# Kernel optimization log

Hardware: AMD Instinct MI355X
Metric: run time of the kernel (lower is better)

## Reference

```python
import jax, jax.numpy as jnp
import numpy as np

N, E, G = 50000, 1600000, 64
XDIM, HID, NF, NG, GDIM, NL = 32, 128, 128, 50, 16, 6
CUTOFF = 10.0
SHID = 64
EPS = 1e-5

_offset = jnp.linspace(0.0, CUTOFF, NG)
_coeff = -0.5 / float((CUTOFF / (NG - 1)) ** 2)


def _bn(h, g, b):
    m = h.mean(axis=0)
    v = h.var(axis=0)
    return (h - m) * jax.lax.rsqrt(v + EPS) * g + b


def setup_inputs() -> dict:
    key = jax.random.key(0)
    ks = jax.random.split(key, 48)

    def w(k, shape):
        fan = shape[-2] if len(shape) >= 2 else shape[-1]
        return (jax.random.normal(k, shape, jnp.float32) / np.sqrt(fan)).astype(jnp.float32)

    inp = {
        "x": jax.random.normal(ks[0], (N, XDIM), jnp.float32),
        "edge_index": jax.random.randint(ks[1], (2, E), 0, N, dtype=jnp.int32).astype(jnp.int64),
        "edge_attr": jax.random.normal(ks[2], (E, 3), jnp.float32),
        "batch": jnp.sort(jax.random.randint(ks[3], (N,), 0, G, dtype=jnp.int32)).astype(jnp.int64),
        "u": jax.random.normal(ks[4], (G, GDIM), jnp.float32),
        # node encoder MLP: lin -> bn -> relu -> lin
        "We1": w(ks[5], (XDIM, HID)), "be1": jnp.zeros(HID), "ge1": jnp.ones(HID), "bte1": jnp.zeros(HID),
        "We2": w(ks[6], (HID, HID)), "be2": jnp.zeros(HID),
        # 6 stacked interactions
        "Wf1": w(ks[7], (NL, NG, NF)), "bf1": jnp.zeros((NL, NF)),
        "Wf2": w(ks[8], (NL, NF, NF)), "bf2": jnp.zeros((NL, NF)),
        "Wd1": w(ks[9], (NL, HID, HID)), "bd1": jnp.zeros((NL, HID)),
        "Wd2": w(ks[10], (NL, HID, HID)), "bd2": jnp.zeros((NL, HID)),
        # global MLP: lin -> bn -> relu -> lin
        "Wg1": w(ks[11], (GDIM, HID)), "bg1": jnp.zeros(HID), "gg1": jnp.ones(HID), "btg1": jnp.zeros(HID),
        "Wg2": w(ks[12], (HID, HID)), "bg2": jnp.zeros(HID),
        # shift predictor: [2*HID, 64, 64, 1]
        "Ws1": w(ks[13], (2 * HID, SHID)), "bs1": jnp.zeros(SHID), "gs1": jnp.ones(SHID), "bts1": jnp.zeros(SHID),
        "Ws2": w(ks[14], (SHID, SHID)), "bs2": jnp.zeros(SHID), "gs2": jnp.ones(SHID), "bts2": jnp.zeros(SHID),
        "Ws3": w(ks[15], (SHID, 1)), "bs3": jnp.zeros(1),
    }
    return inp


def reference(x, edge_index, edge_attr, batch, u,
              We1, be1, ge1, bte1, We2, be2,
              Wf1, bf1, Wf2, bf2, Wd1, bd1, Wd2, bd2,
              Wg1, bg1, gg1, btg1, Wg2, bg2,
              Ws1, bs1, gs1, bts1, Ws2, bs2, gs2, bts2, Ws3, bs3):
    row = edge_index[0]  # source j
    col = edge_index[1]  # target i

    # node encoder
    h = jax.nn.relu(_bn(x @ We1 + be1, ge1, bte1)) @ We2 + be2  # [N,HID]

    # gaussian smearing of edge lengths
    d = jnp.linalg.norm(edge_attr, axis=1)  # [E]
    ea = jnp.exp(_coeff * jnp.square(d[:, None] - _offset[None, :]))  # [E,NG]

    for l in range(NL):
        W = jax.nn.relu(ea @ Wf1[l] + bf1[l]) @ Wf2[l] + bf2[l]  # [E,NF]
        msg = h[row] * W                                          # gather + elementwise
        agg = jax.ops.segment_sum(msg, col, num_segments=N)       # scatter-add
        h = h + (jax.nn.relu(agg @ Wd1[l] + bd1[l]) @ Wd2[l] + bd2[l])

    # global MLP
    u_p = jax.nn.relu(_bn(u @ Wg1 + bg1, gg1, btg1)) @ Wg2 + bg2  # [G,HID]

    # shift predictor on [h, u_p[batch]]
    s = jnp.concatenate([h, u_p[batch]], axis=1)  # [N,2*HID]
    s = jax.nn.relu(_bn(s @ Ws1 + bs1, gs1, bts1))
    s = jax.nn.relu(_bn(s @ Ws2 + bs2, gs2, bts2))
    shifts = s @ Ws3 + bs3  # [N,1]
    return shifts, h, ea, u_p
```

## Files before the change

kernel.cpp:

```cpp
#include <hip/hip_runtime.h>

#define NN 50000
#define NE 1600000
#define NGR 64
#define XD 32
#define HID 128
#define NF 128
#define NG 50
#define GD 16
#define NL 6
#define SH 64
#define EPSF 1e-5f
#define TBL 4096
#define INVSTEP 320.0f

typedef __bf16 bf16_t;
typedef bf16_t bf16x8 __attribute__((ext_vector_type(8)));
typedef float f32x4 __attribute__((ext_vector_type(4)));

__device__ __forceinline__ unsigned pack_bf2(float a, float b) {
  unsigned short ua = __builtin_bit_cast(unsigned short, (bf16_t)a);
  unsigned short ub = __builtin_bit_cast(unsigned short, (bf16_t)b);
  return (unsigned)ua | ((unsigned)ub << 16);
}
__device__ __forceinline__ float bflo(unsigned u) { return __uint_as_float(u << 16); }
__device__ __forceinline__ float bfhi(unsigned u) { return __uint_as_float(u & 0xffff0000u); }
__device__ __forceinline__ float blerp(unsigned u, float fr) {
  float w0 = bflo(u), w1 = bfhi(u);
  return fmaf(fr, w1 - w0, w0);
}

__global__ __launch_bounds__(256) void k_hist(const int* __restrict__ col,
                                              int* __restrict__ hist) {
  for (int e = blockIdx.x * 256 + threadIdx.x; e < NE; e += gridDim.x * 256)
    atomicAdd(&hist[col[e]], 1);
}

__global__ __launch_bounds__(1024) void k_scan(int* __restrict__ hist,
                                               int* __restrict__ rowptr) {
  const int tid = threadIdx.x;
  const int CH = 49;
  const int base = tid * CH;
  int s = 0;
  for (int i = 0; i < CH; ++i) {
    int idx = base + i;
    if (idx < NN) s += hist[idx];
  }
  __shared__ int part[1024];
  part[tid] = s;
  __syncthreads();
  for (int off = 1; off < 1024; off <<= 1) {
    int v = (tid >= off) ? part[tid - off] : 0;
    __syncthreads();
    part[tid] += v;
    __syncthreads();
  }
  int run = part[tid] - s;
  for (int i = 0; i < CH; ++i) {
    int idx = base + i;
    if (idx < NN) {
      int c = hist[idx];
      rowptr[idx] = run;
      hist[idx] = run;
      run += c;
    }
  }
  if (tid == 0) rowptr[NN] = NE;
}

__global__ __launch_bounds__(256) void k_scatter2(const int* __restrict__ col,
    const int* __restrict__ row, const float* __restrict__ eattr,
    int* __restrict__ cursor, uint2* __restrict__ metap) {
  for (int e = blockIdx.x * 256 + threadIdx.x; e < NE; e += gridDim.x * 256) {
    float ax = eattr[(size_t)e * 3], ay = eattr[(size_t)e * 3 + 1], az = eattr[(size_t)e * 3 + 2];
    float d = sqrtf(ax * ax + ay * ay + az * az);
    float tt = fminf(d * INVSTEP, (float)(TBL - 2) + 0.999f);
    int id = (int)tt;
    int c = col[e];
    int pos = atomicAdd(&cursor[c], 1);
    unsigned mw = ((unsigned)row[e] << 16) | ((unsigned)id << 4) | (unsigned)(c & 15);
    metap[pos] = make_uint2(mw, __float_as_uint(tt - (float)id));
  }
}

__global__ __launch_bounds__(128) void k_tabbuild3(
    const float* __restrict__ Wf1, const float* __restrict__ bf1,
    const float* __restrict__ Wf2, const float* __restrict__ bf2,
    unsigned int* __restrict__ tabp) {
  const int bid = blockIdx.x;
  const int l = bid / (TBL / 8);
  const int t0 = (bid - l * (TBL / 8)) * 8;
  const int c = threadIdx.x;
  __shared__ float g_s[9][NG];
  __shared__ float f1_s[9][NF];
  for (int i = c; i < 9 * NG; i += 128) {
    int kk = i / NG, g = i - kk * NG;
    int t = min(t0 + kk, TBL - 1);
    float d = (float)t * (1.0f / INVSTEP);
    float z = d - 0.2040816327f * (float)g;
    g_s[kk][g] = expf(-12.005f * z * z);
  }
  __syncthreads();
  const float* W1 = Wf1 + (size_t)l * NG * NF;
  float f1r[9];
#pragma unroll
  for (int kk = 0; kk < 9; ++kk) f1r[kk] = bf1[(size_t)l * NF + c];
  for (int g = 0; g < NG; ++g) {
    float w = W1[g * NF + c];
#pragma unroll
    for (int kk = 0; kk < 9; ++kk) f1r[kk] = fmaf(g_s[kk][g], w, f1r[kk]);
  }
#pragma unroll
  for (int kk = 0; kk < 9; ++kk) f1_s[kk][c] = fmaxf(f1r[kk], 0.f);
  __syncthreads();
  const float* W2 = Wf2 + (size_t)l * NF * NF;
  float outr[9];
#pragma unroll
  for (int kk = 0; kk < 9; ++kk) outr[kk] = bf2[(size_t)l * NF + c];
  for (int k = 0; k < NF; ++k) {
    float w = W2[k * NF + c];
#pragma unroll
    for (int kk = 0; kk < 9; ++kk) outr[kk] = fmaf(f1_s[kk][k], w, outr[kk]);
  }
#pragma unroll
  for (int kk = 0; kk < 8; ++kk)
    tabp[((size_t)l * TBL + t0 + kk) * NF + c] = pack_bf2(outr[kk], outr[kk + 1]);
}

__global__ __launch_bounds__(256) void k_prepw(const float* __restrict__ Wd1,
    const float* __restrict__ Wd2,
    bf16_t* __restrict__ Wd1Thi, bf16_t* __restrict__ Wd1Tlo,
    bf16_t* __restrict__ Wd2Thi, bf16_t* __restrict__ Wd2Tlo) {
  const int S1 = NL * 128 * 128;
  int idx = blockIdx.x * 256 + threadIdx.x;
  if (idx < 2 * S1) {
    int which = idx / S1;
    int jj = idx - which * S1;
    int l = jj / (128 * 128);
    int r = jj - l * (128 * 128);
    int c = r >> 7, k = r & 127;
    const float* W = (which == 0) ? Wd1 : Wd2;
    float v = W[(size_t)l * 128 * 128 + (size_t)k * 128 + c];
    bf16_t hv = (bf16_t)v;
    bf16_t lv = (bf16_t)(v - (float)hv);
    if (which == 0) { Wd1Thi[jj] = hv; Wd1Tlo[jj] = lv; }
    else            { Wd2Thi[jj] = hv; Wd2Tlo[jj] = lv; }
  }
}

__global__ __launch_bounds__(256) void k_enc1(const float* __restrict__ x,
    const float* __restrict__ We1, const float* __restrict__ be1,
    float* __restrict__ t, float* __restrict__ stats) {
  int c = threadIdx.x & 127;
  int half = threadIdx.x >> 7;
  float b = be1[c];
  float psum = 0.f, psq = 0.f;
  for (int n = blockIdx.x * 2 + half; n < NN; n += gridDim.x * 2) {
    const float* xr = x + (size_t)n * XD;
    float v = b;
#pragma unroll
    for (int k = 0; k < XD; ++k) v = fmaf(xr[k], We1[k * HID + c], v);
    t[(size_t)n * HID + c] = v;
    psum += v; psq += v * v;
  }
  __shared__ float s0[256], s1[256];
  s0[threadIdx.x] = psum; s1[threadIdx.x] = psq;
  __syncthreads();
  if (threadIdx.x < 128) {
    atomicAdd(&stats[threadIdx.x], s0[threadIdx.x] + s0[threadIdx.x + 128]);
    atomicAdd(&stats[128 + threadIdx.x], s1[threadIdx.x] + s1[threadIdx.x + 128]);
  }
}

__global__ __launch_bounds__(128) void k_bn_fin(const float* __restrict__ gamma,
    const float* __restrict__ beta, float* __restrict__ stats, int C, float invn) {
  int c = threadIdx.x;
  if (c < C) {
    float mean = stats[c] * invn;
    float var = stats[128 + c] * invn - mean * mean;
    float a = gamma[c] * rsqrtf(var + EPSF);
    stats[256 + c] = a;
    stats[384 + c] = beta[c] - mean * a;
  }
}

__global__ __launch_bounds__(128) void k_enc2(const float* __restrict__ t,
    const float* __restrict__ stats, const float* __restrict__ We2,
    const float* __restrict__ be2, float* __restrict__ h,
    unsigned int* __restrict__ hbf) {
  __shared__ float r[HID];
  int c = threadIdx.x;
  float a = stats[256 + c], b = stats[384 + c];
  float bias = be2[c];
  for (int n = blockIdx.x; n < NN; n += gridDim.x) {
    float v = fmaf(t[(size_t)n * HID + c], a, b);
    r[c] = fmaxf(v, 0.f);
    __syncthreads();
    float acc = bias;
#pragma unroll 8
    for (int k = 0; k < HID; ++k) acc = fmaf(r[k], We2[k * HID + c], acc);
    h[(size_t)n * HID + c] = acc;
    float o = __shfl_down(acc, 1);
    if ((c & 1) == 0) hbf[(size_t)n * 64 + (c >> 1)] = pack_bf2(acc, o);
    __syncthreads();
  }
}

__global__ __launch_bounds__(256) void k_smear(const float* __restrict__ eattr,
    float* __restrict__ ea) {
  int idx = blockIdx.x * 256 + threadIdx.x;
  if (idx >= NE * (NG / 2)) return;
  int e = idx / (NG / 2);
  int g0 = (idx - e * (NG / 2)) * 2;
  float ax = eattr[(size_t)e * 3], ay = eattr[(size_t)e * 3 + 1], az = eattr[(size_t)e * 3 + 2];
  float d = sqrtf(ax * ax + ay * ay + az * az);
  float z0 = d - 0.2040816327f * (float)g0;
  float z1 = d - 0.2040816327f * (float)(g0 + 1);
  float2 v = make_float2(__expf(-12.005f * z0 * z0), __expf(-12.005f * z1 * z1));
  *(float2*)(ea + (size_t)e * NG + g0) = v;
}

__global__ __launch_bounds__(256) void k_layer(
    const uint2* __restrict__ metap, const int* __restrict__ rowptr,
    const float* __restrict__ hin, const unsigned int* __restrict__ hbf,
    const unsigned int* __restrict__ tabp,
    const bf16_t* __restrict__ Wd1Thi, const bf16_t* __restrict__ Wd1Tlo,
    const bf16_t* __restrict__ Wd2Thi, const bf16_t* __restrict__ Wd2Tlo,
    const float* __restrict__ bd1, const float* __restrict__ bd2,
    float* __restrict__ hout, unsigned int* __restrict__ hbfo) {
  __shared__ __align__(16) char up[8704];
  float (*agg_s)[HID] = (float(*)[HID])up;
  bf16_t (*t1hi)[136] = (bf16_t(*)[136])up;
  bf16_t (*t1lo)[136] = (bf16_t(*)[136])(up + 4352);
  __shared__ __align__(16) bf16_t ahi_s[16][136];
  __shared__ __align__(16) bf16_t alo_s[16][136];

  const int tid = threadIdx.x;
  const int lane = tid & 63;
  const int w = tid >> 6;
  const int half = lane >> 5;
  const int c0 = (lane & 31) * 4;
  const int hoff = c0 >> 1;
  const int nb = blockIdx.x * 16;
  const int eS = rowptr[nb], eE = rowptr[nb + 16];

  for (int i = tid; i < 16 * HID; i += 256) ((float*)agg_s)[i] = 0.f;
  __syncthreads();

  {
    const int Q = (eE - eS + 3) >> 2;
    int e = eS + w * Q;
    const int wE = min(e + Q, eE);

    float a0 = 0.f, a1 = 0.f, a2 = 0.f, a3 = 0.f;
    int cur = -1;

    auto flush = [&]() {
      if (cur >= 0) {
        atomicAdd(&agg_s[cur][c0], a0);
        atomicAdd(&agg_s[cur][c0 + 1], a1);
        atomicAdd(&agg_s[cur][c0 + 2], a2);
        atomicAdd(&agg_s[cur][c0 + 3], a3);
      }
    };
    auto pbody = [&](const uint2& m, const uint2& hv, const uint4& tv) {
      float fr = __uint_as_float(m.y);
      int dst = m.x & 0xF;
      float m0 = blerp(tv.x, fr) * bflo(hv.x);
      float m1 = blerp(tv.y, fr) * bfhi(hv.x);
      float m2 = blerp(tv.z, fr) * bflo(hv.y);
      float m3 = blerp(tv.w, fr) * bfhi(hv.y);
      if (dst != cur) {
        flush();
        cur = dst; a0 = m0; a1 = m1; a2 = m2; a3 = m3;
      } else {
        a0 += m0; a1 += m1; a2 += m2; a3 += m3;
      }
    };
    auto loadd = [&](const uint2& m, uint2& hv, uint4& tv) {
      hv = *(const uint2*)(hbf + (size_t)(m.x >> 16) * 64 + hoff);
      tv = *(const uint4*)(tabp + (size_t)((m.x >> 4) & 0xFFFu) * HID + c0);
    };

    if (wE - e >= 8) {
      uint2 m0a = metap[e + half], m0b = metap[e + 2 + half];
      uint2 hv0a, hv0b; uint4 tv0a, tv0b;
      loadd(m0a, hv0a, tv0a); loadd(m0b, hv0b, tv0b);
      int ep = e + 4;
      uint2 m1a = metap[ep + half], m1b = metap[ep + 2 + half];
      while (true) {
        const bool more = (ep + 8 <= wE);
        uint2 hv1a, hv1b; uint4 tv1a, tv1b;
        loadd(m1a, hv1a, tv1a); loadd(m1b, hv1b, tv1b);
        uint2 m2a, m2b;
        if (more) { m2a = metap[ep + 4 + half]; m2b = metap[ep + 6 + half]; }
        pbody(m0a, hv0a, tv0a);
        pbody(m0b, hv0b, tv0b);
        if (!more) {
          pbody(m1a, hv1a, tv1a);
          pbody(m1b, hv1b, tv1b);
          ep += 4;
          break;
        }
        m0a = m1a; m0b = m1b;
        hv0a = hv1a; hv0b = hv1b; tv0a = tv1a; tv0b = tv1b;
        m1a = m2a; m1b = m2b;
        ep += 4;
      }
      e = ep;
    }
    for (; e < wE; e += 2) {
      int le = e + half;
      bool valid = le < wE;
      uint2 m = metap[valid ? le : (wE - 1)];
      uint2 hv; uint4 tv;
      loadd(m, hv, tv);
      if (valid) pbody(m, hv, tv);
    }
    flush();
  }
  __syncthreads();

  for (int i = tid; i < 16 * 128; i += 256) {
    int r = i >> 7, k = i & 127;
    float v = agg_s[r][k];
    bf16_t hv = (bf16_t)v;
    ahi_s[r][k] = hv;
    alo_s[r][k] = (bf16_t)(v - (float)hv);
  }
  __syncthreads();

  const int lm = lane & 15;
  const int lk = lane >> 4;
  const int colb = w * 32;
  const int k0base = lk * 8;

  f32x4 acc1g[2];
  acc1g[0] = (f32x4){0.f, 0.f, 0.f, 0.f};
  acc1g[1] = (f32x4){0.f, 0.f, 0.f, 0.f};
#pragma unroll
  for (int s = 0; s < 4; ++s) {
    int k0 = s * 32 + k0base;
    bf16x8 Ahi = *(const bf16x8*)&ahi_s[lm][k0];
    bf16x8 Alo = *(const bf16x8*)&alo_s[lm][k0];
#pragma unroll
    for (int cf = 0; cf < 2; ++cf) {
      int cc = colb + cf * 16 + lm;
      bf16x8 Bh = *(const bf16x8*)(Wd1Thi + (size_t)cc * 128 + k0);
      bf16x8 Bl = *(const bf16x8*)(Wd1Tlo + (size_t)cc * 128 + k0);
      acc1g[cf] = __builtin_amdgcn_mfma_f32_16x16x32_bf16(Ahi, Bh, acc1g[cf], 0, 0, 0);
      acc1g[cf] = __builtin_amdgcn_mfma_f32_16x16x32_bf16(Ahi, Bl, acc1g[cf], 0, 0, 0);
      acc1g[cf] = __builtin_amdgcn_mfma_f32_16x16x32_bf16(Alo, Bh, acc1g[cf], 0, 0, 0);
    }
  }
#pragma unroll
  for (int cf = 0; cf < 2; ++cf) {
    int cc = colb + cf * 16 + lm;
    float bias1 = bd1[cc];
#pragma unroll
    for (int j = 0; j < 4; ++j) {
      int r = lk * 4 + j;
      float v = fmaxf(acc1g[cf][j] + bias1, 0.f);
      bf16_t hv = (bf16_t)v;
      t1hi[r][cc] = hv;
      t1lo[r][cc] = (bf16_t)(v - (float)hv);
    }
  }
  __syncthreads();

  f32x4 acc2g[2];
  acc2g[0] = (f32x4){0.f, 0.f, 0.f, 0.f};
  acc2g[1] = (f32x4){0.f, 0.f, 0.f, 0.f};
#pragma unroll
  for (int s = 0; s < 4; ++s) {
    int k0 = s * 32 + k0base;
    bf16x8 Ahi = *(const bf16x8*)&t1hi[lm][k0];
    bf16x8 Alo = *(const bf16x8*)&t1lo[lm][k0];
#pragma unroll
    for (int cf = 0; cf < 2; ++cf) {
      int cc = colb + cf * 16 + lm;
      bf16x8 Bh = *(const bf16x8*)(Wd2Thi + (size_t)cc * 128 + k0);
      bf16x8 Bl = *(const bf16x8*)(Wd2Tlo + (size_t)cc * 128 + k0);
      acc2g[cf] = __builtin_amdgcn_mfma_f32_16x16x32_bf16(Ahi, Bh, acc2g[cf], 0, 0, 0);
      acc2g[cf] = __builtin_amdgcn_mfma_f32_16x16x32_bf16(Ahi, Bl, acc2g[cf], 0, 0, 0);
      acc2g[cf] = __builtin_amdgcn_mfma_f32_16x16x32_bf16(Alo, Bh, acc2g[cf], 0, 0, 0);
    }
  }
#pragma unroll
  for (int cf = 0; cf < 2; ++cf) {
    int cc = colb + cf * 16 + lm;
    float bias2 = bd2[cc];
#pragma unroll
    for (int j = 0; j < 4; ++j) {
      int r = nb + lk * 4 + j;
      float val = hin[(size_t)r * HID + cc] + acc2g[cf][j] + bias2;
      hout[(size_t)r * HID + cc] = val;
      float o = __shfl_xor(val, 1);
      if ((lm & 1) == 0) hbfo[(size_t)r * 64 + (cc >> 1)] = pack_bf2(val, o);
    }
  }
}

__global__ __launch_bounds__(128) void k_global(const float* __restrict__ u,
    const float* __restrict__ Wg1, const float* __restrict__ bg1,
    const float* __restrict__ gg1, const float* __restrict__ btg1,
    const float* __restrict__ Wg2, const float* __restrict__ bg2,
    float* __restrict__ u_p) {
  __shared__ float t_s[NGR][HID];
  int c = threadIdx.x;
  for (int g = 0; g < NGR; ++g) {
    float v = bg1[c];
#pragma unroll
    for (int k = 0; k < GD; ++k) v = fmaf(u[(size_t)g * GD + k], Wg1[k * HID + c], v);
    t_s[g][c] = v;
  }
  float sum = 0.f, sq = 0.f;
  for (int g = 0; g < NGR; ++g) { float v = t_s[g][c]; sum += v; sq += v * v; }
  float mean = sum * (1.f / NGR);
  float var = sq * (1.f / NGR) - mean * mean;
  float a = gg1[c] * rsqrtf(var + EPSF);
  float b = btg1[c] - mean * a;
  for (int g = 0; g < NGR; ++g) t_s[g][c] = fmaxf(fmaf(t_s[g][c], a, b), 0.f);
  __syncthreads();
  for (int g = 0; g < NGR; ++g) {
    float acc = bg2[c];
#pragma unroll 8
    for (int k = 0; k < HID; ++k) acc = fmaf(t_s[g][k], Wg2[k * HID + c], acc);
    u_p[(size_t)g * HID + c] = acc;
  }
}

__global__ __launch_bounds__(256) void k_shift1(
    const float* __restrict__ h, const float* __restrict__ u_p,
    const int* __restrict__ batch, const float* __restrict__ Ws1,
    const float* __restrict__ bs1, float* __restrict__ t1, float* __restrict__ stats) {
  __shared__ float s_in[16][2 * HID];
  const int c = threadIdx.x & 63;
  const int ng = threadIdx.x >> 6;
  float psum = 0.f, psq = 0.f;
  for (int tile = blockIdx.x; tile < NN / 16; tile += gridDim.x) {
    const int nb = tile * 16;
    for (int i = threadIdx.x; i < 16 * HID; i += 256) {
      int ln = i >> 7, k = i & 127;
      s_in[ln][k] = h[(size_t)(nb + ln) * HID + k];
      s_in[ln][HID + k] = u_p[(size_t)batch[nb + ln] * HID + k];
    }
    __syncthreads();
    float acc[4];
#pragma unroll
    for (int j = 0; j < 4; ++j) acc[j] = bs1[c];
    for (int k = 0; k < 2 * HID; ++k) {
      float w = Ws1[k * SH + c];
#pragma unroll
      for (int j = 0; j < 4; ++j) acc[j] = fmaf(s_in[ng * 4 + j][k], w, acc[j]);
    }
#pragma unroll
    for (int j = 0; j < 4; ++j) {
      t1[(size_t)(nb + ng * 4 + j) * SH + c] = acc[j];
      psum += acc[j]; psq += acc[j] * acc[j];
    }
    __syncthreads();
  }
  __shared__ float rs[256], rq[256];
  rs[threadIdx.x] = psum; rq[threadIdx.x] = psq;
  __syncthreads();
  if (threadIdx.x < 64) {
    int c2 = threadIdx.x;
    atomicAdd(&stats[c2], rs[c2] + rs[c2 + 64] + rs[c2 + 128] + rs[c2 + 192]);
    atomicAdd(&stats[128 + c2], rq[c2] + rq[c2 + 64] + rq[c2 + 128] + rq[c2 + 192]);
  }
}

__global__ __launch_bounds__(256) void k_shift2(
    const float* __restrict__ t1, float* __restrict__ stats,
    const float* __restrict__ Ws2, const float* __restrict__ bs2,
    float* __restrict__ t2) {
  __shared__ float r_s[16][SH];
  const int c = threadIdx.x & 63;
  const int ng = threadIdx.x >> 6;
  float psum = 0.f, psq = 0.f;
  for (int tile = blockIdx.x; tile < NN / 16; tile += gridDim.x) {
    const int nb = tile * 16;
    for (int i = threadIdx.x; i < 16 * SH; i += 256) {
      int ln = i >> 6, k = i & 63;
      float v = fmaf(t1[(size_t)(nb + ln) * SH + k], stats[256 + k], stats[384 + k]);
      r_s[ln][k] = fmaxf(v, 0.f);
    }
    __syncthreads();
    float acc[4];
#pragma unroll
    for (int j = 0; j < 4; ++j) acc[j] = bs2[c];
    for (int k = 0; k < SH; ++k) {
      float w = Ws2[k * SH + c];
#pragma unroll
      for (int j = 0; j < 4; ++j) acc[j] = fmaf(r_s[ng * 4 + j][k], w, acc[j]);
    }
#pragma unroll
    for (int j = 0; j < 4; ++j) {
      t2[(size_t)(nb + ng * 4 + j) * SH + c] = acc[j];
      psum += acc[j]; psq += acc[j] * acc[j];
    }
    __syncthreads();
  }
  __shared__ float rs[256], rq[256];
  rs[threadIdx.x] = psum; rq[threadIdx.x] = psq;
  __syncthreads();
  if (threadIdx.x < 64) {
    int c2 = threadIdx.x;
    atomicAdd(&stats[c2], rs[c2] + rs[c2 + 64] + rs[c2 + 128] + rs[c2 + 192]);
    atomicAdd(&stats[128 + c2], rq[c2] + rq[c2 + 64] + rq[c2 + 128] + rq[c2 + 192]);
  }
}

__global__ __launch_bounds__(256) void k_shift3(
    const float* __restrict__ t2, const float* __restrict__ stats,
    const float* __restrict__ Ws3, const float* __restrict__ bs3,
    float* __restrict__ shifts) {
  int lane = threadIdx.x & 63;
  int n = blockIdx.x * 4 + (threadIdx.x >> 6);
  if (n >= NN) return;
  float a = stats[256 + lane], b = stats[384 + lane];
  float r = fmaxf(fmaf(t2[(size_t)n * SH + lane], a, b), 0.f);
  float v = r * Ws3[lane];
#pragma unroll
  for (int off = 32; off; off >>= 1) v += __shfl_down(v, off);
  if (lane == 0) shifts[n] = v + bs3[0];
}

extern "C" void kernel_launch(void* const* d_in, const int* in_sizes, int n_in,
                              void* d_out, int out_size, void* d_ws, size_t ws_size,
                              hipStream_t stream) {
  const float* x     = (const float*)d_in[0];
  const int*   ei    = (const int*)d_in[1];
  const float* eattr = (const float*)d_in[2];
  const int*   batch = (const int*)d_in[3];
  const float* u     = (const float*)d_in[4];
  const float* We1 = (const float*)d_in[5];  const float* be1 = (const float*)d_in[6];
  const float* ge1 = (const float*)d_in[7];  const float* bte1 = (const float*)d_in[8];
  const float* We2 = (const float*)d_in[9];  const float* be2 = (const float*)d_in[10];
  const float* Wf1 = (const float*)d_in[11]; const float* bf1 = (const float*)d_in[12];
  const float* Wf2 = (const float*)d_in[13]; const float* bf2 = (const float*)d_in[14];
  const float* Wd1 = (const float*)d_in[15]; const float* bd1 = (const float*)d_in[16];
  const float* Wd2 = (const float*)d_in[17]; const float* bd2 = (const float*)d_in[18];
  const float* Wg1 = (const float*)d_in[19]; const float* bg1 = (const float*)d_in[20];
  const float* gg1 = (const float*)d_in[21]; const float* btg1 = (const float*)d_in[22];
  const float* Wg2 = (const float*)d_in[23]; const float* bg2 = (const float*)d_in[24];
  const float* Ws1 = (const float*)d_in[25]; const float* bs1 = (const float*)d_in[26];
  const float* gs1 = (const float*)d_in[27]; const float* bts1 = (const float*)d_in[28];
  const float* Ws2 = (const float*)d_in[29]; const float* bs2 = (const float*)d_in[30];
  const float* gs2 = (const float*)d_in[31]; const float* bts2 = (const float*)d_in[32];
  const float* Ws3 = (const float*)d_in[33]; const float* bs3 = (const float*)d_in[34];

  float* out    = (float*)d_out;
  float* shifts = out;
  float* h      = out + NN;
  float* ea     = out + NN + NN * HID;
  float* u_p    = out + NN + NN * HID + (size_t)NE * NG;

  char* wsb = (char*)d_ws;
  size_t off = 0;
  auto alloc = [&](size_t bytes) { void* p = wsb + off; off = (off + bytes + 255) & ~(size_t)255; return p; };
  float*  stats    = (float*)alloc(512 * sizeof(float));
  int*    hist     = (int*)alloc((size_t)NN * sizeof(int));
  int*    rowptr   = (int*)alloc((size_t)(NN + 1) * sizeof(int));
  uint2*  metap    = (uint2*)alloc((size_t)NE * sizeof(uint2));
  unsigned int* tabp = (unsigned int*)alloc((size_t)NL * TBL * HID * sizeof(unsigned int));
  bf16_t* Wd1Thi   = (bf16_t*)alloc((size_t)NL * 128 * 128 * sizeof(bf16_t));
  bf16_t* Wd1Tlo   = (bf16_t*)alloc((size_t)NL * 128 * 128 * sizeof(bf16_t));
  bf16_t* Wd2Thi   = (bf16_t*)alloc((size_t)NL * 128 * 128 * sizeof(bf16_t));
  bf16_t* Wd2Tlo   = (bf16_t*)alloc((size_t)NL * 128 * 128 * sizeof(bf16_t));
  float*  hwork    = (float*)alloc((size_t)NN * HID * sizeof(float));
  unsigned int* hbfA = (unsigned int*)alloc((size_t)NN * 64 * sizeof(unsigned int));
  unsigned int* hbfB = (unsigned int*)alloc((size_t)NN * 64 * sizeof(unsigned int));
  float*  buf1     = (float*)alloc((size_t)NN * HID * sizeof(float));
  float* t1 = buf1;
  float* t2 = buf1 + (size_t)NN * SH;

  const int* row = ei;
  const int* col = ei + NE;

  hipMemsetAsync(hist, 0, (size_t)NN * sizeof(int), stream);
  k_hist<<<512, 256, 0, stream>>>(col, hist);
  k_scan<<<1, 1024, 0, stream>>>(hist, rowptr);
  k_scatter2<<<512, 256, 0, stream>>>(col, row, eattr, hist, metap);
  k_tabbuild3<<<NL * (TBL / 8), 128, 0, stream>>>(Wf1, bf1, Wf2, bf2, tabp);
  k_prepw<<<(2 * NL * 128 * 128 + 255) / 256, 256, 0, stream>>>(
      Wd1, Wd2, Wd1Thi, Wd1Tlo, Wd2Thi, Wd2Tlo);

  hipMemsetAsync(stats, 0, 256 * sizeof(float), stream);
  k_enc1<<<512, 256, 0, stream>>>(x, We1, be1, buf1, stats);
  k_bn_fin<<<1, 128, 0, stream>>>(ge1, bte1, stats, 128, 1.f / NN);
  k_enc2<<<2048, 128, 0, stream>>>(buf1, stats, We2, be2, h, hbfA);

  k_smear<<<(NE * (NG / 2) + 255) / 256, 256, 0, stream>>>(eattr, ea);

  for (int l = 0; l < NL; ++l) {
    const float* hi = (l & 1) ? hwork : h;
    float*       ho = (l & 1) ? h : hwork;
    const unsigned int* bi = (l & 1) ? hbfB : hbfA;
    unsigned int*       bo = (l & 1) ? hbfA : hbfB;
    k_layer<<<NN / 16, 256, 0, stream>>>(
        metap, rowptr, hi, bi, tabp + (size_t)l * TBL * HID,
        Wd1Thi + (size_t)l * 128 * 128, Wd1Tlo + (size_t)l * 128 * 128,
        Wd2Thi + (size_t)l * 128 * 128, Wd2Tlo + (size_t)l * 128 * 128,
        bd1 + (size_t)l * HID, bd2 + (size_t)l * HID, ho, bo);
  }

  k_global<<<1, 128, 0, stream>>>(u, Wg1, bg1, gg1, btg1, Wg2, bg2, u_p);

  hipMemsetAsync(stats, 0, 256 * sizeof(float), stream);
  k_shift1<<<1024, 256, 0, stream>>>(h, u_p, batch, Ws1, bs1, t1, stats);
  k_bn_fin<<<1, 128, 0, stream>>>(gs1, bts1, stats, 64, 1.f / NN);
  hipMemsetAsync(stats, 0, 256 * sizeof(float), stream);
  k_shift2<<<1024, 256, 0, stream>>>(t1, stats, Ws2, bs2, t2);
  k_bn_fin<<<1, 128, 0, stream>>>(gs2, bts2, stats, 64, 1.f / NN);
  k_shift3<<<(NN + 3) / 4, 256, 0, stream>>>(t2, stats, Ws3, bs3, shifts);
}
```

Baseline: 1.721 ms.

## Move encoder and shift-predictor dense layers to split-bf16 MFMA

Replaces the scalar FMA matmuls in the node encoder second layer and the two shift-predictor layers with MFMA 16x16x32 bf16 kernels. These use a hi/lo bf16 split (three MFMAs per step) to keep close to fp32 accuracy. A new prep kernel transposes and splits We2, Ws1 and Ws2 once per call. The launches change from grid-stride loops to one block per 16-node tile, and BN statistics are reduced with wave shuffles before the atomics. The added costs are an extra launch for weight prep, more atomics because there are more blocks, and a small rounding change from the split-bf16 arithmetic.

```diff
diff --git a/kernel.cpp b/kernel.cpp
--- a/kernel.cpp
+++ b/kernel.cpp
@@ -148,6 +148,35 @@
   }
 }
 
+__global__ __launch_bounds__(256) void k_prepw2(const float* __restrict__ We2,
+    const float* __restrict__ Ws1, const float* __restrict__ Ws2,
+    bf16_t* __restrict__ We2Thi, bf16_t* __restrict__ We2Tlo,
+    bf16_t* __restrict__ Ws1Thi, bf16_t* __restrict__ Ws1Tlo,
+    bf16_t* __restrict__ Ws2Thi, bf16_t* __restrict__ Ws2Tlo) {
+  const int S0 = 128 * 128;
+  const int S1 = 64 * 256;
+  const int S2 = 64 * 64;
+  int idx = blockIdx.x * 256 + threadIdx.x;
+  if (idx < S0) {
+    int c = idx >> 7, k = idx & 127;
+    float v = We2[k * 128 + c];
+    bf16_t hv = (bf16_t)v;
+    We2Thi[idx] = hv; We2Tlo[idx] = (bf16_t)(v - (float)hv);
+  } else if (idx < S0 + S1) {
+    int j = idx - S0;
+    int c = j >> 8, k = j & 255;
+    float v = Ws1[k * 64 + c];
+    bf16_t hv = (bf16_t)v;
+    Ws1Thi[j] = hv; Ws1Tlo[j] = (bf16_t)(v - (float)hv);
+  } else if (idx < S0 + S1 + S2) {
+    int j = idx - S0 - S1;
+    int c = j >> 6, k = j & 63;
+    float v = Ws2[k * 64 + c];
+    bf16_t hv = (bf16_t)v;
+    Ws2Thi[j] = hv; Ws2Tlo[j] = (bf16_t)(v - (float)hv);
+  }
+}
+
 __global__ __launch_bounds__(256) void k_enc1(const float* __restrict__ x,
     const float* __restrict__ We1, const float* __restrict__ be1,
     float* __restrict__ t, float* __restrict__ stats) {
@@ -184,25 +213,54 @@
   }
 }
 
-__global__ __launch_bounds__(128) void k_enc2(const float* __restrict__ t,
-    const float* __restrict__ stats, const float* __restrict__ We2,
+__global__ __launch_bounds__(256) void k_enc2m(const float* __restrict__ t,
+    const float* __restrict__ stats,
+    const bf16_t* __restrict__ We2Thi, const bf16_t* __restrict__ We2Tlo,
     const float* __restrict__ be2, float* __restrict__ h,
     unsigned int* __restrict__ hbf) {
-  __shared__ float r[HID];
-  int c = threadIdx.x;
-  float a = stats[256 + c], b = stats[384 + c];
-  float bias = be2[c];
-  for (int n = blockIdx.x; n < NN; n += gridDim.x) {
-    float v = fmaf(t[(size_t)n * HID + c], a, b);
-    r[c] = fmaxf(v, 0.f);
-    __syncthreads();
-    float acc = bias;
-#pragma unroll 8
-    for (int k = 0; k < HID; ++k) acc = fmaf(r[k], We2[k * HID + c], acc);
-    h[(size_t)n * HID + c] = acc;
-    float o = __shfl_down(acc, 1);
-    if ((c & 1) == 0) hbf[(size_t)n * 64 + (c >> 1)] = pack_bf2(acc, o);
-    __syncthreads();
+  __shared__ __align__(16) bf16_t rhi[16][136];
+  __shared__ __align__(16) bf16_t rlo[16][136];
+  const int tid = threadIdx.x, lane = tid & 63, w = tid >> 6;
+  const int lm = lane & 15, lk = lane >> 4;
+  const int nb = blockIdx.x * 16;
+  for (int i = tid; i < 16 * 128; i += 256) {
+    int r = i >> 7, k = i & 127;
+    float v = fmaxf(fmaf(t[(size_t)(nb + r) * HID + k], stats[256 + k], stats[384 + k]), 0.f);
+    bf16_t hv = (bf16_t)v;
+    rhi[r][k] = hv; rlo[r][k] = (bf16_t)(v - (float)hv);
+  }
+  __syncthreads();
+  const int colb = w * 32, k0base = lk * 8;
+  f32x4 acc[2];
+  acc[0] = (f32x4){0.f, 0.f, 0.f, 0.f};
+  acc[1] = (f32x4){0.f, 0.f, 0.f, 0.f};
+#pragma unroll
+  for (int s = 0; s < 4; ++s) {
+    int k0 = s * 32 + k0base;
+    bf16x8 Ahi = *(const bf16x8*)&rhi[lm][k0];
+    bf16x8 Alo = *(const bf16x8*)&rlo[lm][k0];
+#pragma unroll
+    for (int cf = 0; cf < 2; ++cf) {
+      int cc = colb + cf * 16 + lm;
+      bf16x8 Bh = *(const bf16x8*)(We2Thi + (size_t)cc * 128 + k0);
+      bf16x8 Bl = *(const bf16x8*)(We2Tlo + (size_t)cc * 128 + k0);
+      acc[cf] = __builtin_amdgcn_mfma_f32_16x16x32_bf16(Ahi, Bh, acc[cf], 0, 0, 0);
+      acc[cf] = __builtin_amdgcn_mfma_f32_16x16x32_bf16(Ahi, Bl, acc[cf], 0, 0, 0);
+      acc[cf] = __builtin_amdgcn_mfma_f32_16x16x32_bf16(Alo, Bh, acc[cf], 0, 0, 0);
+    }
+  }
+#pragma unroll
+  for (int cf = 0; cf < 2; ++cf) {
+    int cc = colb + cf * 16 + lm;
+    float bias = be2[cc];
+#pragma unroll
+    for (int j = 0; j < 4; ++j) {
+      int r = nb + lk * 4 + j;
+      float val = acc[cf][j] + bias;
+      h[(size_t)r * HID + cc] = val;
+      float o = __shfl_xor(val, 1);
+      if ((lm & 1) == 0) hbf[(size_t)r * 64 + (cc >> 1)] = pack_bf2(val, o);
+    }
   }
 }
 
@@ -430,85 +488,98 @@
   }
 }
 
-__global__ __launch_bounds__(256) void k_shift1(
+__global__ __launch_bounds__(256) void k_shift1m(
     const float* __restrict__ h, const float* __restrict__ u_p,
-    const int* __restrict__ batch, const float* __restrict__ Ws1,
-    const float* __restrict__ bs1, float* __restrict__ t1, float* __restrict__ stats) {
-  __shared__ float s_in[16][2 * HID];
-  const int c = threadIdx.x & 63;
-  const int ng = threadIdx.x >> 6;
+    const int* __restrict__ batch,
+    const bf16_t* __restrict__ Ws1Thi, const bf16_t* __restrict__ Ws1Tlo,
+    const float* __restrict__ bs1, float* __restrict__ t1,
+    float* __restrict__ stats) {
+  __shared__ __align__(16) bf16_t shi[16][264];
+  __shared__ __align__(16) bf16_t slo[16][264];
+  const int tid = threadIdx.x, lane = tid & 63, w = tid >> 6;
+  const int lm = lane & 15, lk = lane >> 4;
+  const int nb = blockIdx.x * 16;
+  for (int i = tid; i < 16 * 128; i += 256) {
+    int ln = i >> 7, k = i & 127;
+    float v1 = h[(size_t)(nb + ln) * HID + k];
+    float v2 = u_p[(size_t)batch[nb + ln] * HID + k];
+    bf16_t h1 = (bf16_t)v1;
+    shi[ln][k] = h1; slo[ln][k] = (bf16_t)(v1 - (float)h1);
+    bf16_t h2 = (bf16_t)v2;
+    shi[ln][128 + k] = h2; slo[ln][128 + k] = (bf16_t)(v2 - (float)h2);
+  }
+  __syncthreads();
+  const int cc = w * 16 + lm;
+  f32x4 acc = (f32x4){0.f, 0.f, 0.f, 0.f};
+#pragma unroll
+  for (int s = 0; s < 8; ++s) {
+    int k0 = s * 32 + lk * 8;
+    bf16x8 Ahi = *(const bf16x8*)&shi[lm][k0];
+    bf16x8 Alo = *(const bf16x8*)&slo[lm][k0];
+    bf16x8 Bh = *(const bf16x8*)(Ws1Thi + (size_t)cc * 256 + k0);
+    bf16x8 Bl = *(const bf16x8*)(Ws1Tlo + (size_t)cc * 256 + k0);
+    acc = __builtin_amdgcn_mfma_f32_16x16x32_bf16(Ahi, Bh, acc, 0, 0, 0);
+    acc = __builtin_amdgcn_mfma_f32_16x16x32_bf16(Ahi, Bl, acc, 0, 0, 0);
+    acc = __builtin_amdgcn_mfma_f32_16x16x32_bf16(Alo, Bh, acc, 0, 0, 0);
+  }
+  float bias = bs1[cc];
   float psum = 0.f, psq = 0.f;
-  for (int tile = blockIdx.x; tile < NN / 16; tile += gridDim.x) {
-    const int nb = tile * 16;
-    for (int i = threadIdx.x; i < 16 * HID; i += 256) {
-      int ln = i >> 7, k = i & 127;
-      s_in[ln][k] = h[(size_t)(nb + ln) * HID + k];
-      s_in[ln][HID + k] = u_p[(size_t)batch[nb + ln] * HID + k];
-    }
-    __syncthreads();
-    float acc[4];
-#pragma unroll
-    for (int j = 0; j < 4; ++j) acc[j] = bs1[c];
-    for (int k = 0; k < 2 * HID; ++k) {
-      float w = Ws1[k * SH + c];
-#pragma unroll
-      for (int j = 0; j < 4; ++j) acc[j] = fmaf(s_in[ng * 4 + j][k], w, acc[j]);
-    }
-#pragma unroll
-    for (int j = 0; j < 4; ++j) {
-      t1[(size_t)(nb + ng * 4 + j) * SH + c] = acc[j];
-      psum += acc[j]; psq += acc[j] * acc[j];
-    }
-    __syncthreads();
-  }
-  __shared__ float rs[256], rq[256];
-  rs[threadIdx.x] = psum; rq[threadIdx.x] = psq;
-  __syncthreads();
-  if (threadIdx.x < 64) {
-    int c2 = threadIdx.x;
-    atomicAdd(&stats[c2], rs[c2] + rs[c2 + 64] + rs[c2 + 128] + rs[c2 + 192]);
-    atomicAdd(&stats[128 + c2], rq[c2] + rq[c2 + 64] + rq[c2 + 128] + rq[c2 + 192]);
-  }
-}
-
-__global__ __launch_bounds__(256) void k_shift2(
+#pragma unroll
+  for (int j = 0; j < 4; ++j) {
+    float val = acc[j] + bias;
+    t1[(size_t)(nb + lk * 4 + j) * SH + cc] = val;
+    psum += val; psq += val * val;
+  }
+  psum += __shfl_xor(psum, 16); psum += __shfl_xor(psum, 32);
+  psq  += __shfl_xor(psq, 16);  psq  += __shfl_xor(psq, 32);
+  if (lk == 0) {
+    atomicAdd(&stats[cc], psum);
+    atomicAdd(&stats[128 + cc], psq);
+  }
+}
+
+__global__ __launch_bounds__(256) void k_shift2m(
     const float* __restrict__ t1, float* __restrict__ stats,
-    const float* __restrict__ Ws2, const float* __restrict__ bs2,
-    float* __restrict__ t2) {
-  __shared__ float r_s[16][SH];
-  const int c = threadIdx.x & 63;
-  const int ng = threadIdx.x >> 6;
+    const bf16_t* __restrict__ Ws2Thi, const bf16_t* __restrict__ Ws2Tlo,
+    const float* __restrict__ bs2, float* __restrict__ t2) {
+  __shared__ __align__(16) bf16_t rhi[16][72];
+  __shared__ __align__(16) bf16_t rlo[16][72];
+  const int tid = threadIdx.x, lane = tid & 63, w = tid >> 6;
+  const int lm = lane & 15, lk = lane >> 4;
+  const int nb = blockIdx.x * 16;
+  for (int i = tid; i < 16 * 64; i += 256) {
+    int ln = i >> 6, k = i & 63;
+    float v = fmaxf(fmaf(t1[(size_t)(nb + ln) * SH + k], stats[256 + k], stats[384 + k]), 0.f);
+    bf16_t hv = (bf16_t)v;
+    rhi[ln][k] = hv; rlo[ln][k] = (bf16_t)(v - (float)hv);
+  }
+  __syncthreads();
+  const int cc = w * 16 + lm;
+  f32x4 acc = (f32x4){0.f, 0.f, 0.f, 0.f};
+#pragma unroll
+  for (int s = 0; s < 2; ++s) {
+    int k0 = s * 32 + lk * 8;
+    bf16x8 Ahi = *(const bf16x8*)&rhi[lm][k0];
+    bf16x8 Alo = *(const bf16x8*)&rlo[lm][k0];
+    bf16x8 Bh = *(const bf16x8*)(Ws2Thi + (size_t)cc * 64 + k0);
+    bf16x8 Bl = *(const bf16x8*)(Ws2Tlo + (size_t)cc * 64 + k0);
+    acc = __builtin_amdgcn_mfma_f32_16x16x32_bf16(Ahi, Bh, acc, 0, 0, 0);
+    acc = __builtin_amdgcn_mfma_f32_16x16x32_bf16(Ahi, Bl, acc, 0, 0, 0);
+    acc = __builtin_amdgcn_mfma_f32_16x16x32_bf16(Alo, Bh, acc, 0, 0, 0);
+  }
+  float bias = bs2[cc];
   float psum = 0.f, psq = 0.f;
-  for (int tile = blockIdx.x; tile < NN / 16; tile += gridDim.x) {
-    const int nb = tile * 16;
-    for (int i = threadIdx.x; i < 16 * SH; i += 256) {
-      int ln = i >> 6, k = i & 63;
-      float v = fmaf(t1[(size_t)(nb + ln) * SH + k], stats[256 + k], stats[384 + k]);
-      r_s[ln][k] = fmaxf(v, 0.f);
-    }
-    __syncthreads();
-    float acc[4];
-#pragma unroll
-    for (int j = 0; j < 4; ++j) acc[j] = bs2[c];
-    for (int k = 0; k < SH; ++k) {
-      float w = Ws2[k * SH + c];
-#pragma unroll
-      for (int j = 0; j < 4; ++j) acc[j] = fmaf(r_s[ng * 4 + j][k], w, acc[j]);
-    }
-#pragma unroll
-    for (int j = 0; j < 4; ++j) {
-      t2[(size_t)(nb + ng * 4 + j) * SH + c] = acc[j];
-      psum += acc[j]; psq += acc[j] * acc[j];
-    }
-    __syncthreads();
-  }
-  __shared__ float rs[256], rq[256];
-  rs[threadIdx.x] = psum; rq[threadIdx.x] = psq;
-  __syncthreads();
-  if (threadIdx.x < 64) {
-    int c2 = threadIdx.x;
-    atomicAdd(&stats[c2], rs[c2] + rs[c2 + 64] + rs[c2 + 128] + rs[c2 + 192]);
-    atomicAdd(&stats[128 + c2], rq[c2] + rq[c2 + 64] + rq[c2 + 128] + rq[c2 + 192]);
+#pragma unroll
+  for (int j = 0; j < 4; ++j) {
+    float val = acc[j] + bias;
+    t2[(size_t)(nb + lk * 4 + j) * SH + cc] = val;
+    psum += val; psq += val * val;
+  }
+  psum += __shfl_xor(psum, 16); psum += __shfl_xor(psum, 32);
+  psq  += __shfl_xor(psq, 16);  psq  += __shfl_xor(psq, 32);
+  if (lk == 0) {
+    atomicAdd(&stats[cc], psum);
+    atomicAdd(&stats[128 + cc], psq);
   }
 }
 
@@ -569,6 +640,12 @@
   bf16_t* Wd1Tlo   = (bf16_t*)alloc((size_t)NL * 128 * 128 * sizeof(bf16_t));
   bf16_t* Wd2Thi   = (bf16_t*)alloc((size_t)NL * 128 * 128 * sizeof(bf16_t));
   bf16_t* Wd2Tlo   = (bf16_t*)alloc((size_t)NL * 128 * 128 * sizeof(bf16_t));
+  bf16_t* We2Thi   = (bf16_t*)alloc((size_t)128 * 128 * sizeof(bf16_t));
+  bf16_t* We2Tlo   = (bf16_t*)alloc((size_t)128 * 128 * sizeof(bf16_t));
+  bf16_t* Ws1Thi   = (bf16_t*)alloc((size_t)64 * 256 * sizeof(bf16_t));
+  bf16_t* Ws1Tlo   = (bf16_t*)alloc((size_t)64 * 256 * sizeof(bf16_t));
+  bf16_t* Ws2Thi   = (bf16_t*)alloc((size_t)64 * 64 * sizeof(bf16_t));
+  bf16_t* Ws2Tlo   = (bf16_t*)alloc((size_t)64 * 64 * sizeof(bf16_t));
   float*  hwork    = (float*)alloc((size_t)NN * HID * sizeof(float));
   unsigned int* hbfA = (unsigned int*)alloc((size_t)NN * 64 * sizeof(unsigned int));
   unsigned int* hbfB = (unsigned int*)alloc((size_t)NN * 64 * sizeof(unsigned int));
@@ -586,11 +663,13 @@
   k_tabbuild3<<<NL * (TBL / 8), 128, 0, stream>>>(Wf1, bf1, Wf2, bf2, tabp);
   k_prepw<<<(2 * NL * 128 * 128 + 255) / 256, 256, 0, stream>>>(
       Wd1, Wd2, Wd1Thi, Wd1Tlo, Wd2Thi, Wd2Tlo);
+  k_prepw2<<<(128 * 128 + 64 * 256 + 64 * 64 + 255) / 256, 256, 0, stream>>>(
+      We2, Ws1, Ws2, We2Thi, We2Tlo, Ws1Thi, Ws1Tlo, Ws2Thi, Ws2Tlo);
 
   hipMemsetAsync(stats, 0, 256 * sizeof(float), stream);
   k_enc1<<<512, 256, 0, stream>>>(x, We1, be1, buf1, stats);
   k_bn_fin<<<1, 128, 0, stream>>>(ge1, bte1, stats, 128, 1.f / NN);
-  k_enc2<<<2048, 128, 0, stream>>>(buf1, stats, We2, be2, h, hbfA);
+  k_enc2m<<<NN / 16, 256, 0, stream>>>(buf1, stats, We2Thi, We2Tlo, be2, h, hbfA);
 
   k_smear<<<(NE * (NG / 2) + 255) / 256, 256, 0, stream>>>(eattr, ea);
 
@@ -609,10 +688,10 @@
   k_global<<<1, 128, 0, stream>>>(u, Wg1, bg1, gg1, btg1, Wg2, bg2, u_p);
 
   hipMemsetAsync(stats, 0, 256 * sizeof(float), stream);
-  k_shift1<<<1024, 256, 0, stream>>>(h, u_p, batch, Ws1, bs1, t1, stats);
+  k_shift1m<<<NN / 16, 256, 0, stream>>>(h, u_p, batch, Ws1Thi, Ws1Tlo, bs1, t1, stats);
   k_bn_fin<<<1, 128, 0, stream>>>(gs1, bts1, stats, 64, 1.f / NN);
   hipMemsetAsync(stats, 0, 256 * sizeof(float), stream);
-  k_shift2<<<1024, 256, 0, stream>>>(t1, stats, Ws2, bs2, t2);
+  k_shift2m<<<NN / 16, 256, 0, stream>>>(t1, stats, Ws2Thi, Ws2Tlo, bs2, t2);
   k_bn_fin<<<1, 128, 0, stream>>>(gs2, bts2, stats, 64, 1.f / NN);
   k_shift3<<<(NN + 3) / 4, 256, 0, stream>>>(t2, stats, Ws3, bs3, shifts);
 }
```

Measured after the change: 1.723 ms. About the same (+0.1%).
